# Kernel optimization log

Hardware: AMD Instinct MI355X
Metric: run time of the kernel (lower is better)

## Reference

```python
import jax, jax.numpy as jnp
import numpy as np

E = 256   # embed_dim
H = 8     # num_heads
D = E // H  # head_dim = 32
L = 1024  # seq len (Q_len == K_len == V_len)


def setup_inputs() -> dict:
    key = jax.random.key(0)
    ks = jax.random.split(key, 10)
    f = lambda k, s: jax.random.normal(k, s, dtype=jnp.float32)
    return {
        "V": f(ks[0], (L, E)),
        "K": f(ks[1], (L, E)),
        "Q": f(ks[2], (L, E)),
        # genomic-style coordinates, strictly positive
        "position": jax.random.uniform(ks[3], (L,), dtype=jnp.float32) * 1e5,
        "Wq": f(ks[4], (E, E)) * 0.02,
        "Wk": f(ks[5], (E, E)) * 0.02,
        "Wv": f(ks[6], (E, E)) * 0.02,
        "Wr": f(ks[7], (E, 1)) * 0.02,   # K_relative_linear weight [out=E, in=1]
        "Wo": f(ks[8], (E, E)) * 0.02,
        "bo": jnp.zeros((E,), jnp.float32),
    }


def reference(V, K, Q, position, Wq, Wk, Wv, Wr, Wo, bo):
    Lq = Q.shape[0]
    # projections (nn.Linear: x @ W.T), split into heads -> (L, H, D)
    q = (Q @ Wq.T).reshape(Lq, H, D)
    k = (K @ Wk.T).reshape(Lq, H, D)
    v = (V @ Wv.T).reshape(Lq, H, D)

    # relative position scalar per (q, k) pair: log(|p_q - p_k| + 1)
    rel = jnp.log(jnp.abs(position[:, None] - position[None, :]) + 1.0)  # (L, L)

    # K_relative_linear maps scalar rel -> (H, D); the einsum
    # 'nqhd,nhqjd->nhqj' then factorizes exactly as:
    #   sum_d Q[q,h,d] * rel[q,j] * Wr[h,d] = (Q . Wr)[h,q] * rel[q,j]
    # so we avoid materializing the (H, L, L, D) tensor while computing
    # mathematically identical results.
    Wr_h = Wr[:, 0].reshape(H, D)                    # (H, D)
    coeff = jnp.einsum('qhd,hd->hq', q, Wr_h)        # (H, L)

    energy = jnp.einsum('qhd,khd->hqk', q, k)        # (H, L, L)
    energy = energy + coeff[:, :, None] * rel[None, :, :]

    attn = jax.nn.softmax(energy / np.float32(E) ** 0.5, axis=2)
    out = jnp.einsum('hqk,khd->qhd', attn, v).reshape(Lq, E)
    out = out @ Wo.T + bo
    return out
```

## Files before the change

kernel.cpp:

```cpp
#include <hip/hip_runtime.h>
#include <math.h>

#define EDIM 256
#define LDIM 1024
#define HDIM 8
#define DDIM 32

typedef __attribute__((ext_vector_type(8))) short short8;
typedef __attribute__((ext_vector_type(4))) short short4v;
typedef __attribute__((ext_vector_type(4))) float f32x4;

__device__ inline unsigned short bf16h(float x) {
    unsigned u = __float_as_uint(x);
    return (unsigned short)((u + 0x7fff + ((u >> 16) & 1)) >> 16);
}
__device__ inline float bf16tof(unsigned short h) {
    return __uint_as_float(((unsigned)h) << 16);
}
__device__ inline void split8(const float4& a, const float4& b, short8& hi, short8& lo) {
    float v[8] = {a.x,a.y,a.z,a.w, b.x,b.y,b.z,b.w};
    #pragma unroll
    for (int j = 0; j < 8; ++j) {
        unsigned short hh = bf16h(v[j]);
        hi[j] = (short)hh;
        lo[j] = (short)bf16h(v[j] - bf16tof(hh));
    }
}

__global__ __launch_bounds__(256) void convertw_kernel(
    const float* __restrict__ Wq, const float* __restrict__ Wk,
    const float* __restrict__ Wv, const float* __restrict__ Wo,
    short* __restrict__ Wqh, short* __restrict__ Wql,
    short* __restrict__ Wkh, short* __restrict__ Wkl,
    short* __restrict__ Wvh, short* __restrict__ Wvl,
    short* __restrict__ Woh, short* __restrict__ Wol)
{
    const int z = blockIdx.y;
    const float* src; short* dh; short* dl;
    switch (z) {
        case 0: src = Wq; dh = Wqh; dl = Wql; break;
        case 1: src = Wk; dh = Wkh; dl = Wkl; break;
        case 2: src = Wv; dh = Wvh; dl = Wvl; break;
        default: src = Wo; dh = Woh; dl = Wol; break;
    }
    const int idx = (blockIdx.x * 256 + threadIdx.x) * 8;
    float4 a = *(const float4*)(src + idx);
    float4 b = *(const float4*)(src + idx + 4);
    short8 hi, lo;
    split8(a, b, hi, lo);
    *(short8*)&dh[idx] = hi;
    *(short8*)&dl[idx] = lo;
}

__global__ __launch_bounds__(128) void proj_kernel(
    const float* __restrict__ Q, const float* __restrict__ K, const float* __restrict__ V,
    const short* __restrict__ Wqh, const short* __restrict__ Wql,
    const short* __restrict__ Wkh, const short* __restrict__ Wkl,
    const short* __restrict__ Wvh, const short* __restrict__ Wvl,
    const float* __restrict__ Wr,
    float* __restrict__ qT, float* __restrict__ kT, float* __restrict__ vT,
    float* __restrict__ coeff)
{
    const int z = blockIdx.z;
    const float* __restrict__ X  = (z == 0) ? Q : (z == 1) ? K : V;
    const short* __restrict__ Wh = (z == 0) ? Wqh : (z == 1) ? Wkh : Wvh;
    const short* __restrict__ Wl = (z == 0) ? Wql : (z == 1) ? Wkl : Wvl;
    float* __restrict__ dst      = (z == 0) ? qT : (z == 1) ? kT : vT;

    const int n0 = blockIdx.x * 32;
    const int o0 = blockIdx.y * 64;
    const int wave = threadIdx.x >> 6;
    const int lane = threadIdx.x & 63;
    const int n16  = lane & 15;
    const int quad = lane >> 4;

    const int mrow = n0 + wave*16 + n16;

    f32x4 acc[4];
    #pragma unroll
    for (int t4 = 0; t4 < 4; ++t4) acc[t4] = (f32x4){0.f,0.f,0.f,0.f};

    #pragma unroll 2
    for (int kb = 0; kb < EDIM; kb += 32) {
        const float* xp = X + mrow*EDIM + kb + quad*8;
        float4 a0 = *(const float4*)xp;
        float4 a1 = *(const float4*)(xp + 4);
        short8 ah, al;
        split8(a0, a1, ah, al);
        #pragma unroll
        for (int t4 = 0; t4 < 4; ++t4) {
            const int orow = o0 + 16*t4 + n16;
            short8 bh = *(const short8*)&Wh[orow*EDIM + kb + quad*8];
            short8 bl = *(const short8*)&Wl[orow*EDIM + kb + quad*8];
            acc[t4] = __builtin_amdgcn_mfma_f32_16x16x32_bf16(al, bh, acc[t4], 0, 0, 0);
            acc[t4] = __builtin_amdgcn_mfma_f32_16x16x32_bf16(ah, bl, acc[t4], 0, 0, 0);
            acc[t4] = __builtin_amdgcn_mfma_f32_16x16x32_bf16(ah, bh, acc[t4], 0, 0, 0);
        }
    }

    #pragma unroll
    for (int t4 = 0; t4 < 4; ++t4) {
        const int o = o0 + 16*t4 + n16;
        const int h = o >> 5, d = o & 31;
        #pragma unroll
        for (int i = 0; i < 4; ++i) {
            const int r = n0 + wave*16 + quad*4 + i;
            dst[h*(LDIM*DDIM) + r*DDIM + d] = acc[t4][i];
        }
    }

    if (z == 0) {
        float wr[4];
        #pragma unroll
        for (int t4 = 0; t4 < 4; ++t4) wr[t4] = Wr[o0 + 16*t4 + n16];
        const int h0 = o0 >> 5;
        #pragma unroll
        for (int i = 0; i < 4; ++i) {
            float c0 = acc[0][i]*wr[0] + acc[1][i]*wr[1];
            float c1 = acc[2][i]*wr[2] + acc[3][i]*wr[3];
            #pragma unroll
            for (int off = 1; off < 16; off <<= 1) {
                c0 += __shfl_xor(c0, off, 64);
                c1 += __shfl_xor(c1, off, 64);
            }
            if (n16 == 0) {
                const int r = n0 + wave*16 + quad*4 + i;
                coeff[h0*LDIM + r]     = c0;
                coeff[(h0+1)*LDIM + r] = c1;
            }
        }
    }
}

__global__ __launch_bounds__(256, 4) void attn_kernel(
    const float* __restrict__ qT, const float* __restrict__ kT, const float* __restrict__ vT,
    const float* __restrict__ coeff, const float* __restrict__ pos,
    float* __restrict__ Op, float* __restrict__ Mp, float* __restrict__ Lp, int nkt)
{
    const int h   = blockIdx.y;
    const int q0  = blockIdx.x * 64;
    const int p   = blockIdx.z;
    const int kt0 = p * nkt * 64;
    const int tid  = threadIdx.x;
    const int wave = tid >> 6;
    const int lane = tid & 63;
    const int n    = lane & 15;
    const int quad = lane >> 4;
    const int qs0  = wave * 16;

    __shared__ __align__(16) short khi[4*64*8];
    __shared__ __align__(16) short klo[4*64*8];
    __shared__ float vs[64][36];
    __shared__ float ps_t[64][68];
    __shared__ float alph[64];
    __shared__ float pk[64];

    short8 qhi, qlo;
    {
        const float* qp = qT + (h*LDIM + q0 + qs0 + n) * DDIM + quad*8;
        float4 qa = *(const float4*)qp;
        float4 qb = *(const float4*)(qp + 4);
        split8(qa, qb, qhi, qlo);
    }

    float pq[4], cq[4];
    #pragma unroll
    for (int i = 0; i < 4; ++i) {
        const int r = q0 + qs0 + 4*quad + i;
        pq[i] = pos[r];
        cq[i] = coeff[h*LDIM + r] * 0.0625f;
    }

    float m[4], l[4];
    #pragma unroll
    for (int i = 0; i < 4; ++i) { m[i] = -INFINITY; l[i] = 0.f; }

    const int pr0 = (tid >> 4) * 4;
    const int dg2 = (tid & 15) * 2;
    float o[4][2];
    #pragma unroll
    for (int i = 0; i < 4; ++i) { o[i][0] = 0.f; o[i][1] = 0.f; }

    const int cS = tid >> 2;
    const int dq = tid & 3;
    const int lane2 = (cS & 15) | (dq << 4);
    const int gS = cS >> 4;

    float4 k0c, k1c, v0c, v1c; float pkc = 0.f;
    {
        const float* kp = kT + (h*LDIM + kt0 + cS) * DDIM + dq*8;
        k0c = *(const float4*)kp; k1c = *(const float4*)(kp + 4);
        const float* vp = vT + (h*LDIM + kt0 + cS) * DDIM + dq*8;
        v0c = *(const float4*)vp; v1c = *(const float4*)(vp + 4);
        if (tid < 64) pkc = pos[kt0 + tid];
    }

    for (int t = 0; t < nkt; ++t) {
        __syncthreads();

        {
            short8 hi8, lo8;
            split8(k0c, k1c, hi8, lo8);
            *((short8*)&khi[(gS*64 + lane2)*8]) = hi8;
            *((short8*)&klo[(gS*64 + lane2)*8]) = lo8;
            *(float4*)&vs[cS][dq*8]     = v0c;
            *(float4*)&vs[cS][dq*8 + 4] = v1c;
            if (tid < 64) pk[tid] = pkc;
        }

        float4 k0n, k1n, v0n, v1n; float pkn = 0.f;
        if (t + 1 < nkt) {
            const int kt = kt0 + (t+1) * 64;
            const float* kp = kT + (h*LDIM + kt + cS) * DDIM + dq*8;
            k0n = *(const float4*)kp; k1n = *(const float4*)(kp + 4);
            const float* vp = vT + (h*LDIM + kt + cS) * DDIM + dq*8;
            v0n = *(const float4*)vp; v1n = *(const float4*)(vp + 4);
            if (tid < 64) pkn = pos[kt + tid];
        }
        __syncthreads();

        f32x4 Sf[4];
        #pragma unroll
        for (int t4 = 0; t4 < 4; ++t4) {
            short8 bhi = *((const short8*)&khi[(t4*64 + lane)*8]);
            short8 blo = *((const short8*)&klo[(t4*64 + lane)*8]);
            f32x4 acc = {0.f, 0.f, 0.f, 0.f};
            acc = __builtin_amdgcn_mfma_f32_16x16x32_bf16(qlo, bhi, acc, 0, 0, 0);
            acc = __builtin_amdgcn_mfma_f32_16x16x32_bf16(qhi, blo, acc, 0, 0, 0);
            acc = __builtin_amdgcn_mfma_f32_16x16x32_bf16(qhi, bhi, acc, 0, 0, 0);
            Sf[t4] = acc;
        }

        float ev[4][4];
        float rmax[4] = {-INFINITY, -INFINITY, -INFINITY, -INFINITY};
        #pragma unroll
        for (int t4 = 0; t4 < 4; ++t4) {
            const float pkt = pk[16*t4 + n];
            #pragma unroll
            for (int i = 0; i < 4; ++i) {
                float s = fmaf(Sf[t4][i], 0.0625f, cq[i] * __logf(fabsf(pq[i] - pkt) + 1.f));
                ev[t4][i] = s;
                rmax[i] = fmaxf(rmax[i], s);
            }
        }
        #pragma unroll
        for (int off = 1; off < 16; off <<= 1)
            #pragma unroll
            for (int i = 0; i < 4; ++i)
                rmax[i] = fmaxf(rmax[i], __shfl_xor(rmax[i], off, 64));

        float al[4], rsum[4];
        #pragma unroll
        for (int i = 0; i < 4; ++i) {
            const float mn = fmaxf(m[i], rmax[i]);
            al[i] = __expf(m[i] - mn);
            m[i] = mn;
            rsum[i] = 0.f;
        }
        #pragma unroll
        for (int t4 = 0; t4 < 4; ++t4)
            #pragma unroll
            for (int i = 0; i < 4; ++i) {
                float e = __expf(ev[t4][i] - m[i]);
                ev[t4][i] = e;
                rsum[i] += e;
            }
        #pragma unroll
        for (int off = 1; off < 16; off <<= 1)
            #pragma unroll
            for (int i = 0; i < 4; ++i)
                rsum[i] += __shfl_xor(rsum[i], off, 64);
        #pragma unroll
        for (int i = 0; i < 4; ++i) l[i] = l[i]*al[i] + rsum[i];

        if (n == 0) {
            #pragma unroll
            for (int i = 0; i < 4; ++i) alph[qs0 + 4*quad + i] = al[i];
        }
        #pragma unroll
        for (int t4 = 0; t4 < 4; ++t4) {
            float4 w; w.x = ev[t4][0]; w.y = ev[t4][1]; w.z = ev[t4][2]; w.w = ev[t4][3];
            *(float4*)&ps_t[16*t4 + n][qs0 + 4*quad] = w;
        }
        __syncthreads();

        {
            float4 a4 = *(const float4*)&alph[pr0];
            o[0][0]*=a4.x; o[0][1]*=a4.x; o[1][0]*=a4.y; o[1][1]*=a4.y;
            o[2][0]*=a4.z; o[2][1]*=a4.z; o[3][0]*=a4.w; o[3][1]*=a4.w;
        }
        #pragma unroll 4
        for (int c = 0; c < 64; ++c) {
            float4 p4 = *(const float4*)&ps_t[c][pr0];
            float2 v2 = *(const float2*)&vs[c][dg2];
            o[0][0] += p4.x*v2.x; o[0][1] += p4.x*v2.y;
            o[1][0] += p4.y*v2.x; o[1][1] += p4.y*v2.y;
            o[2][0] += p4.z*v2.x; o[2][1] += p4.z*v2.y;
            o[3][0] += p4.w*v2.x; o[3][1] += p4.w*v2.y;
        }

        k0c = k0n; k1c = k1n; v0c = v0n; v1c = v1n; pkc = pkn;
    }

    const int ph = p * HDIM + h;
    #pragma unroll
    for (int i = 0; i < 4; ++i) {
        float2 w; w.x = o[i][0]; w.y = o[i][1];
        *(float2*)(Op + ((size_t)ph*LDIM + q0 + pr0 + i)*DDIM + dg2) = w;
    }
    if (n == 0) {
        #pragma unroll
        for (int i = 0; i < 4; ++i) {
            const int r = q0 + qs0 + 4*quad + i;
            Mp[ph*LDIM + r] = m[i];
            Lp[ph*LDIM + r] = l[i];
        }
    }
}

__global__ __launch_bounds__(256) void combine_kernel(
    const float* __restrict__ Op, const float* __restrict__ Mp, const float* __restrict__ Lp,
    int P, short* __restrict__ Ah, short* __restrict__ Al)
{
    const int idx = blockIdx.x * 256 + threadIdx.x;
    const int n  = idx >> 6;
    const int e4 = (idx & 63) * 4;
    const int h  = e4 >> 5;
    const int d  = e4 & 31;

    float mv[8], lv[8];
    float mx = -INFINITY;
    #pragma unroll
    for (int p = 0; p < 8; ++p) if (p < P) {
        mv[p] = Mp[(p*HDIM + h)*LDIM + n];
        lv[p] = Lp[(p*HDIM + h)*LDIM + n];
        mx = fmaxf(mx, mv[p]);
    }
    float s = 0.f;
    #pragma unroll
    for (int p = 0; p < 8; ++p) if (p < P) {
        float a = __expf(mv[p] - mx);
        mv[p] = a;
        s += a * lv[p];
    }
    const float inv = 1.f / s;

    float x[4] = {0.f, 0.f, 0.f, 0.f};
    #pragma unroll
    for (int p = 0; p < 8; ++p) if (p < P) {
        const float sp = mv[p] * inv;
        float4 xp = *(const float4*)(Op + ((size_t)(p*HDIM + h)*LDIM + n)*DDIM + d);
        x[0] += sp*xp.x; x[1] += sp*xp.y; x[2] += sp*xp.z; x[3] += sp*xp.w;
    }
    short4v hi, lo;
    #pragma unroll
    for (int j = 0; j < 4; ++j) {
        unsigned short hh = bf16h(x[j]);
        hi[j] = (short)hh;
        lo[j] = (short)bf16h(x[j] - bf16tof(hh));
    }
    *(short4v*)&Ah[n*EDIM + e4] = hi;
    *(short4v*)&Al[n*EDIM + e4] = lo;
}

__global__ __launch_bounds__(128) void outproj_kernel(
    const short* __restrict__ Ah, const short* __restrict__ Al,
    const short* __restrict__ Woh, const short* __restrict__ Wol,
    const float* __restrict__ bo, float* __restrict__ out)
{
    const int n0 = blockIdx.x * 32;
    const int o0 = blockIdx.y * 32;
    const int wave = threadIdx.x >> 6;
    const int lane = threadIdx.x & 63;
    const int n16  = lane & 15;
    const int quad = lane >> 4;

    const int mrow = n0 + wave*16 + n16;

    f32x4 acc[2];
    acc[0] = (f32x4){0.f,0.f,0.f,0.f};
    acc[1] = (f32x4){0.f,0.f,0.f,0.f};

    #pragma unroll 2
    for (int kb = 0; kb < EDIM; kb += 32) {
        short8 ah = *(const short8*)&Ah[mrow*EDIM + kb + quad*8];
        short8 al = *(const short8*)&Al[mrow*EDIM + kb + quad*8];
        #pragma unroll
        for (int t2 = 0; t2 < 2; ++t2) {
            const int orow = o0 + 16*t2 + n16;
            short8 bh = *(const short8*)&Woh[orow*EDIM + kb + quad*8];
            short8 bl = *(const short8*)&Wol[orow*EDIM + kb + quad*8];
            acc[t2] = __builtin_amdgcn_mfma_f32_16x16x32_bf16(al, bh, acc[t2], 0, 0, 0);
            acc[t2] = __builtin_amdgcn_mfma_f32_16x16x32_bf16(ah, bl, acc[t2], 0, 0, 0);
            acc[t2] = __builtin_amdgcn_mfma_f32_16x16x32_bf16(ah, bh, acc[t2], 0, 0, 0);
        }
    }

    #pragma unroll
    for (int t2 = 0; t2 < 2; ++t2) {
        const int o = o0 + 16*t2 + n16;
        const float b = bo[o];
        #pragma unroll
        for (int i = 0; i < 4; ++i) {
            const int r = n0 + wave*16 + quad*4 + i;
            out[r*EDIM + o] = acc[t2][i] + b;
        }
    }
}

extern "C" void kernel_launch(void* const* d_in, const int* in_sizes, int n_in,
                              void* d_out, int out_size, void* d_ws, size_t ws_size,
                              hipStream_t stream) {
    const float* V   = (const float*)d_in[0];
    const float* K   = (const float*)d_in[1];
    const float* Q   = (const float*)d_in[2];
    const float* pos = (const float*)d_in[3];
    const float* Wq  = (const float*)d_in[4];
    const float* Wk  = (const float*)d_in[5];
    const float* Wv  = (const float*)d_in[6];
    const float* Wr  = (const float*)d_in[7];
    const float* Wo  = (const float*)d_in[8];
    const float* bo  = (const float*)d_in[9];
    float* out = (float*)d_out;
    float* ws  = (float*)d_ws;

    short* Wqh = (short*)(ws);          short* Wql = (short*)(ws + 32768);
    short* Wkh = (short*)(ws + 65536);  short* Wkl = (short*)(ws + 98304);
    short* Wvh = (short*)(ws + 131072); short* Wvl = (short*)(ws + 163840);
    short* Woh = (short*)(ws + 196608); short* Wol = (short*)(ws + 229376);
    float* qT    = ws + 262144;
    float* kT    = ws + 524288;
    float* vT    = ws + 786432;
    float* coeff = ws + 1048576;
    short* Ah    = (short*)(ws + 1056768);
    short* Al    = (short*)(ws + 1187840);
    float* Op    = ws + 1319040;

    auto need = [](int P) -> size_t {
        return (size_t)(1319040 + P*278528) * 4;
    };
    int P = 2;
    if (ws_size >= need(8)) P = 8;
    else if (ws_size >= need(4)) P = 4;

    float* Mp = Op + (size_t)P * 262144;
    float* Lp = Mp + (size_t)P * 8192;

    convertw_kernel<<<dim3(32, 4),    256, 0, stream>>>(Wq, Wk, Wv, Wo,
        Wqh, Wql, Wkh, Wkl, Wvh, Wvl, Woh, Wol);
    proj_kernel    <<<dim3(32, 4, 3), 128, 0, stream>>>(Q, K, V,
        Wqh, Wql, Wkh, Wkl, Wvh, Wvl, Wr, qT, kT, vT, coeff);
    attn_kernel    <<<dim3(16, 8, P), 256, 0, stream>>>(qT, kT, vT, coeff, pos,
        Op, Mp, Lp, 16 / P);
    combine_kernel <<<dim3(256),      256, 0, stream>>>(Op, Mp, Lp, P, Ah, Al);
    outproj_kernel <<<dim3(32, 8),    128, 0, stream>>>(Ah, Al, Woh, Wol, bo, out);
}
```

Before: 124.4 us.

## Move attention PV product to split-bf16 MFMA and drop weight pre-conversion kernel

The P·V accumulation in the attention kernel moves from scalar FP32 FMAs over shared-memory tiles to three-term split-bf16 MFMA operations. V is staged in LDS as hi/lo bf16 fragments, and P is round-tripped through a row-major LDS buffer. The separate weight-conversion kernel is removed: the projection and output-projection kernels now load FP32 weights and split them inline. The combine kernel writes FP32 output, which reuses the qT buffer. This saves one launch and some memory traffic, at the cost of redundant per-block weight splitting and strided, uncoalesced V loads.

```diff
diff --git a/kernel.cpp b/kernel.cpp
--- a/kernel.cpp
+++ b/kernel.cpp
@@ -7,7 +7,6 @@
 #define DDIM 32
 
 typedef __attribute__((ext_vector_type(8))) short short8;
-typedef __attribute__((ext_vector_type(4))) short short4v;
 typedef __attribute__((ext_vector_type(4))) float f32x4;
 
 __device__ inline unsigned short bf16h(float x) {
@@ -27,45 +26,17 @@
     }
 }
 
-__global__ __launch_bounds__(256) void convertw_kernel(
-    const float* __restrict__ Wq, const float* __restrict__ Wk,
-    const float* __restrict__ Wv, const float* __restrict__ Wo,
-    short* __restrict__ Wqh, short* __restrict__ Wql,
-    short* __restrict__ Wkh, short* __restrict__ Wkl,
-    short* __restrict__ Wvh, short* __restrict__ Wvl,
-    short* __restrict__ Woh, short* __restrict__ Wol)
-{
-    const int z = blockIdx.y;
-    const float* src; short* dh; short* dl;
-    switch (z) {
-        case 0: src = Wq; dh = Wqh; dl = Wql; break;
-        case 1: src = Wk; dh = Wkh; dl = Wkl; break;
-        case 2: src = Wv; dh = Wvh; dl = Wvl; break;
-        default: src = Wo; dh = Woh; dl = Wol; break;
-    }
-    const int idx = (blockIdx.x * 256 + threadIdx.x) * 8;
-    float4 a = *(const float4*)(src + idx);
-    float4 b = *(const float4*)(src + idx + 4);
-    short8 hi, lo;
-    split8(a, b, hi, lo);
-    *(short8*)&dh[idx] = hi;
-    *(short8*)&dl[idx] = lo;
-}
-
 __global__ __launch_bounds__(128) void proj_kernel(
     const float* __restrict__ Q, const float* __restrict__ K, const float* __restrict__ V,
-    const short* __restrict__ Wqh, const short* __restrict__ Wql,
-    const short* __restrict__ Wkh, const short* __restrict__ Wkl,
-    const short* __restrict__ Wvh, const short* __restrict__ Wvl,
+    const float* __restrict__ Wq, const float* __restrict__ Wk, const float* __restrict__ Wv,
     const float* __restrict__ Wr,
     float* __restrict__ qT, float* __restrict__ kT, float* __restrict__ vT,
     float* __restrict__ coeff)
 {
     const int z = blockIdx.z;
-    const float* __restrict__ X  = (z == 0) ? Q : (z == 1) ? K : V;
-    const short* __restrict__ Wh = (z == 0) ? Wqh : (z == 1) ? Wkh : Wvh;
-    const short* __restrict__ Wl = (z == 0) ? Wql : (z == 1) ? Wkl : Wvl;
-    float* __restrict__ dst      = (z == 0) ? qT : (z == 1) ? kT : vT;
+    const float* __restrict__ X   = (z == 0) ? Q : (z == 1) ? K : V;
+    const float* __restrict__ Wfp = (z == 0) ? Wq : (z == 1) ? Wk : Wv;
+    float* __restrict__ dst       = (z == 0) ? qT : (z == 1) ? kT : vT;
 
     const int n0 = blockIdx.x * 32;
     const int o0 = blockIdx.y * 64;
@@ -85,16 +56,19 @@
         const float* xp = X + mrow*EDIM + kb + quad*8;
         float4 a0 = *(const float4*)xp;
         float4 a1 = *(const float4*)(xp + 4);
-        short8 ah, al;
-        split8(a0, a1, ah, al);
+        short8 ah, al8;
+        split8(a0, a1, ah, al8);
         #pragma unroll
         for (int t4 = 0; t4 < 4; ++t4) {
             const int orow = o0 + 16*t4 + n16;
-            short8 bh = *(const short8*)&Wh[orow*EDIM + kb + quad*8];
-            short8 bl = *(const short8*)&Wl[orow*EDIM + kb + quad*8];
-            acc[t4] = __builtin_amdgcn_mfma_f32_16x16x32_bf16(al, bh, acc[t4], 0, 0, 0);
-            acc[t4] = __builtin_amdgcn_mfma_f32_16x16x32_bf16(ah, bl, acc[t4], 0, 0, 0);
-            acc[t4] = __builtin_amdgcn_mfma_f32_16x16x32_bf16(ah, bh, acc[t4], 0, 0, 0);
+            const float* wp = Wfp + orow*EDIM + kb + quad*8;
+            float4 w0 = *(const float4*)wp;
+            float4 w1 = *(const float4*)(wp + 4);
+            short8 bh, bl;
+            split8(w0, w1, bh, bl);
+            acc[t4] = __builtin_amdgcn_mfma_f32_16x16x32_bf16(al8, bh, acc[t4], 0, 0, 0);
+            acc[t4] = __builtin_amdgcn_mfma_f32_16x16x32_bf16(ah,  bl, acc[t4], 0, 0, 0);
+            acc[t4] = __builtin_amdgcn_mfma_f32_16x16x32_bf16(ah,  bh, acc[t4], 0, 0, 0);
         }
     }
 
@@ -150,9 +124,9 @@
 
     __shared__ __align__(16) short khi[4*64*8];
     __shared__ __align__(16) short klo[4*64*8];
-    __shared__ float vs[64][36];
-    __shared__ float ps_t[64][68];
-    __shared__ float alph[64];
+    __shared__ __align__(16) short vhi[4*64*8];
+    __shared__ __align__(16) short vlo[4*64*8];
+    __shared__ float ps2[64*68];
     __shared__ float pk[64];
 
     short8 qhi, qlo;
@@ -175,23 +149,28 @@
     #pragma unroll
     for (int i = 0; i < 4; ++i) { m[i] = -INFINITY; l[i] = 0.f; }
 
-    const int pr0 = (tid >> 4) * 4;
-    const int dg2 = (tid & 15) * 2;
-    float o[4][2];
-    #pragma unroll
-    for (int i = 0; i < 4; ++i) { o[i][0] = 0.f; o[i][1] = 0.f; }
+    f32x4 od[2];
+    od[0] = (f32x4){0.f,0.f,0.f,0.f};
+    od[1] = (f32x4){0.f,0.f,0.f,0.f};
 
     const int cS = tid >> 2;
     const int dq = tid & 3;
     const int lane2 = (cS & 15) | (dq << 4);
     const int gS = cS >> 4;
-
-    float4 k0c, k1c, v0c, v1c; float pkc = 0.f;
+    const int fs  = tid >> 6;
+    const int lv  = tid & 63;
+    const int ccv = fs >> 1;
+    const int tv  = fs & 1;
+    const int cbase = ccv*32 + (lv >> 4)*8;
+    const int dv    = tv*16 + (lv & 15);
+
+    float4 k0c, k1c; float vv[8]; float pkc = 0.f;
     {
         const float* kp = kT + (h*LDIM + kt0 + cS) * DDIM + dq*8;
         k0c = *(const float4*)kp; k1c = *(const float4*)(kp + 4);
-        const float* vp = vT + (h*LDIM + kt0 + cS) * DDIM + dq*8;
-        v0c = *(const float4*)vp; v1c = *(const float4*)(vp + 4);
+        #pragma unroll
+        for (int j = 0; j < 8; ++j)
+            vv[j] = vT[(h*LDIM + kt0 + cbase + j)*DDIM + dv];
         if (tid < 64) pkc = pos[kt0 + tid];
     }
 
@@ -203,18 +182,23 @@
             split8(k0c, k1c, hi8, lo8);
             *((short8*)&khi[(gS*64 + lane2)*8]) = hi8;
             *((short8*)&klo[(gS*64 + lane2)*8]) = lo8;
-            *(float4*)&vs[cS][dq*8]     = v0c;
-            *(float4*)&vs[cS][dq*8 + 4] = v1c;
+            float4 va; va.x = vv[0]; va.y = vv[1]; va.z = vv[2]; va.w = vv[3];
+            float4 vb; vb.x = vv[4]; vb.y = vv[5]; vb.z = vv[6]; vb.w = vv[7];
+            short8 vh8, vl8;
+            split8(va, vb, vh8, vl8);
+            *((short8*)&vhi[(fs*64 + lv)*8]) = vh8;
+            *((short8*)&vlo[(fs*64 + lv)*8]) = vl8;
             if (tid < 64) pk[tid] = pkc;
         }
 
-        float4 k0n, k1n, v0n, v1n; float pkn = 0.f;
+        float4 k0n, k1n; float vvn[8]; float pkn = 0.f;
         if (t + 1 < nkt) {
             const int kt = kt0 + (t+1) * 64;
             const float* kp = kT + (h*LDIM + kt + cS) * DDIM + dq*8;
             k0n = *(const float4*)kp; k1n = *(const float4*)(kp + 4);
-            const float* vp = vT + (h*LDIM + kt + cS) * DDIM + dq*8;
-            v0n = *(const float4*)vp; v1n = *(const float4*)(vp + 4);
+            #pragma unroll
+            for (int j = 0; j < 8; ++j)
+                vvn[j] = vT[(h*LDIM + kt + cbase + j)*DDIM + dv];
             if (tid < 64) pkn = pos[kt + tid];
         }
         __syncthreads();
@@ -273,41 +257,43 @@
         #pragma unroll
         for (int i = 0; i < 4; ++i) l[i] = l[i]*al[i] + rsum[i];
 
-        if (n == 0) {
-            #pragma unroll
-            for (int i = 0; i < 4; ++i) alph[qs0 + 4*quad + i] = al[i];
-        }
-        #pragma unroll
-        for (int t4 = 0; t4 < 4; ++t4) {
-            float4 w; w.x = ev[t4][0]; w.y = ev[t4][1]; w.z = ev[t4][2]; w.w = ev[t4][3];
-            *(float4*)&ps_t[16*t4 + n][qs0 + 4*quad] = w;
-        }
-        __syncthreads();
-
-        {
-            float4 a4 = *(const float4*)&alph[pr0];
-            o[0][0]*=a4.x; o[0][1]*=a4.x; o[1][0]*=a4.y; o[1][1]*=a4.y;
-            o[2][0]*=a4.z; o[2][1]*=a4.z; o[3][0]*=a4.w; o[3][1]*=a4.w;
-        }
-        #pragma unroll 4
-        for (int c = 0; c < 64; ++c) {
-            float4 p4 = *(const float4*)&ps_t[c][pr0];
-            float2 v2 = *(const float2*)&vs[c][dg2];
-            o[0][0] += p4.x*v2.x; o[0][1] += p4.x*v2.y;
-            o[1][0] += p4.y*v2.x; o[1][1] += p4.y*v2.y;
-            o[2][0] += p4.z*v2.x; o[2][1] += p4.z*v2.y;
-            o[3][0] += p4.w*v2.x; o[3][1] += p4.w*v2.y;
-        }
-
-        k0c = k0n; k1c = k1n; v0c = v0n; v1c = v1n; pkc = pkn;
+        #pragma unroll
+        for (int t4 = 0; t4 < 4; ++t4)
+            #pragma unroll
+            for (int i = 0; i < 4; ++i)
+                ps2[(qs0 + 4*quad + i)*68 + 16*t4 + n] = ev[t4][i];
+
+        #pragma unroll
+        for (int i = 0; i < 4; ++i) { od[0][i] *= al[i]; od[1][i] *= al[i]; }
+
+        #pragma unroll
+        for (int cc = 0; cc < 2; ++cc) {
+            const float* pp = &ps2[(qs0 + n)*68 + cc*32 + quad*8];
+            float4 p0 = *(const float4*)pp;
+            float4 p1 = *(const float4*)(pp + 4);
+            short8 phi, plo;
+            split8(p0, p1, phi, plo);
+            #pragma unroll
+            for (int tt = 0; tt < 2; ++tt) {
+                short8 bvh = *((const short8*)&vhi[((cc*2 + tt)*64 + lane)*8]);
+                short8 bvl = *((const short8*)&vlo[((cc*2 + tt)*64 + lane)*8]);
+                od[tt] = __builtin_amdgcn_mfma_f32_16x16x32_bf16(plo, bvh, od[tt], 0, 0, 0);
+                od[tt] = __builtin_amdgcn_mfma_f32_16x16x32_bf16(phi, bvl, od[tt], 0, 0, 0);
+                od[tt] = __builtin_amdgcn_mfma_f32_16x16x32_bf16(phi, bvh, od[tt], 0, 0, 0);
+            }
+        }
+
+        k0c = k0n; k1c = k1n; pkc = pkn;
+        #pragma unroll
+        for (int j = 0; j < 8; ++j) vv[j] = vvn[j];
     }
 
     const int ph = p * HDIM + h;
     #pragma unroll
-    for (int i = 0; i < 4; ++i) {
-        float2 w; w.x = o[i][0]; w.y = o[i][1];
-        *(float2*)(Op + ((size_t)ph*LDIM + q0 + pr0 + i)*DDIM + dg2) = w;
-    }
+    for (int tt = 0; tt < 2; ++tt)
+        #pragma unroll
+        for (int i = 0; i < 4; ++i)
+            Op[((size_t)ph*LDIM + q0 + qs0 + 4*quad + i)*DDIM + tt*16 + n] = od[tt][i];
     if (n == 0) {
         #pragma unroll
         for (int i = 0; i < 4; ++i) {
@@ -320,7 +306,7 @@
 
 __global__ __launch_bounds__(256) void combine_kernel(
     const float* __restrict__ Op, const float* __restrict__ Mp, const float* __restrict__ Lp,
-    int P, short* __restrict__ Ah, short* __restrict__ Al)
+    int P, float* __restrict__ A)
 {
     const int idx = blockIdx.x * 256 + threadIdx.x;
     const int n  = idx >> 6;
@@ -345,27 +331,18 @@
     }
     const float inv = 1.f / s;
 
-    float x[4] = {0.f, 0.f, 0.f, 0.f};
+    float4 x; x.x = x.y = x.z = x.w = 0.f;
     #pragma unroll
     for (int p = 0; p < 8; ++p) if (p < P) {
         const float sp = mv[p] * inv;
         float4 xp = *(const float4*)(Op + ((size_t)(p*HDIM + h)*LDIM + n)*DDIM + d);
-        x[0] += sp*xp.x; x[1] += sp*xp.y; x[2] += sp*xp.z; x[3] += sp*xp.w;
-    }
-    short4v hi, lo;
-    #pragma unroll
-    for (int j = 0; j < 4; ++j) {
-        unsigned short hh = bf16h(x[j]);
-        hi[j] = (short)hh;
-        lo[j] = (short)bf16h(x[j] - bf16tof(hh));
-    }
-    *(short4v*)&Ah[n*EDIM + e4] = hi;
-    *(short4v*)&Al[n*EDIM + e4] = lo;
+        x.x += sp*xp.x; x.y += sp*xp.y; x.z += sp*xp.z; x.w += sp*xp.w;
+    }
+    *(float4*)(A + n*EDIM + e4) = x;
 }
 
 __global__ __launch_bounds__(128) void outproj_kernel(
-    const short* __restrict__ Ah, const short* __restrict__ Al,
-    const short* __restrict__ Woh, const short* __restrict__ Wol,
+    const float* __restrict__ A, const float* __restrict__ Wo,
     const float* __restrict__ bo, float* __restrict__ out)
 {
     const int n0 = blockIdx.x * 32;
@@ -383,16 +360,22 @@
 
     #pragma unroll 2
     for (int kb = 0; kb < EDIM; kb += 32) {
-        short8 ah = *(const short8*)&Ah[mrow*EDIM + kb + quad*8];
-        short8 al = *(const short8*)&Al[mrow*EDIM + kb + quad*8];
+        const float* ap = A + mrow*EDIM + kb + quad*8;
+        float4 a0 = *(const float4*)ap;
+        float4 a1 = *(const float4*)(ap + 4);
+        short8 ah, al8;
+        split8(a0, a1, ah, al8);
         #pragma unroll
         for (int t2 = 0; t2 < 2; ++t2) {
             const int orow = o0 + 16*t2 + n16;
-            short8 bh = *(const short8*)&Woh[orow*EDIM + kb + quad*8];
-            short8 bl = *(const short8*)&Wol[orow*EDIM + kb + quad*8];
-            acc[t2] = __builtin_amdgcn_mfma_f32_16x16x32_bf16(al, bh, acc[t2], 0, 0, 0);
-            acc[t2] = __builtin_amdgcn_mfma_f32_16x16x32_bf16(ah, bl, acc[t2], 0, 0, 0);
-            acc[t2] = __builtin_amdgcn_mfma_f32_16x16x32_bf16(ah, bh, acc[t2], 0, 0, 0);
+            const float* wp = Wo + orow*EDIM + kb + quad*8;
+            float4 w0 = *(const float4*)wp;
+            float4 w1 = *(const float4*)(wp + 4);
+            short8 bh, bl;
+            split8(w0, w1, bh, bl);
+            acc[t2] = __builtin_amdgcn_mfma_f32_16x16x32_bf16(al8, bh, acc[t2], 0, 0, 0);
+            acc[t2] = __builtin_amdgcn_mfma_f32_16x16x32_bf16(ah,  bl, acc[t2], 0, 0, 0);
+            acc[t2] = __builtin_amdgcn_mfma_f32_16x16x32_bf16(ah,  bh, acc[t2], 0, 0, 0);
         }
     }
 
@@ -424,20 +407,14 @@
     float* out = (float*)d_out;
     float* ws  = (float*)d_ws;
 
-    short* Wqh = (short*)(ws);          short* Wql = (short*)(ws + 32768);
-    short* Wkh = (short*)(ws + 65536);  short* Wkl = (short*)(ws + 98304);
-    short* Wvh = (short*)(ws + 131072); short* Wvl = (short*)(ws + 163840);
-    short* Woh = (short*)(ws + 196608); short* Wol = (short*)(ws + 229376);
-    float* qT    = ws + 262144;
-    float* kT    = ws + 524288;
-    float* vT    = ws + 786432;
-    float* coeff = ws + 1048576;
-    short* Ah    = (short*)(ws + 1056768);
-    short* Al    = (short*)(ws + 1187840);
-    float* Op    = ws + 1319040;
+    float* qT    = ws;
+    float* kT    = ws + 262144;
+    float* vT    = ws + 524288;
+    float* coeff = ws + 786432;
+    float* Op    = ws + 794624;
 
     auto need = [](int P) -> size_t {
-        return (size_t)(1319040 + P*278528) * 4;
+        return (size_t)(794624 + P*278528) * 4;
     };
     int P = 2;
     if (ws_size >= need(8)) P = 8;
@@ -445,13 +422,12 @@
 
     float* Mp = Op + (size_t)P * 262144;
     float* Lp = Mp + (size_t)P * 8192;
-
-    convertw_kernel<<<dim3(32, 4),    256, 0, stream>>>(Wq, Wk, Wv, Wo,
-        Wqh, Wql, Wkh, Wkl, Wvh, Wvl, Woh, Wol);
-    proj_kernel    <<<dim3(32, 4, 3), 128, 0, stream>>>(Q, K, V,
-        Wqh, Wql, Wkh, Wkl, Wvh, Wvl, Wr, qT, kT, vT, coeff);
+    float* A  = qT;
+
+    proj_kernel    <<<dim3(32, 4, 3), 128, 0, stream>>>(Q, K, V, Wq, Wk, Wv, Wr,
+                                                        qT, kT, vT, coeff);
     attn_kernel    <<<dim3(16, 8, P), 256, 0, stream>>>(qT, kT, vT, coeff, pos,
-        Op, Mp, Lp, 16 / P);
-    combine_kernel <<<dim3(256),      256, 0, stream>>>(Op, Mp, Lp, P, Ah, Al);
-    outproj_kernel <<<dim3(32, 8),    128, 0, stream>>>(Ah, Al, Woh, Wol, bo, out);
-}
+                                                        Op, Mp, Lp, 16 / P);
+    combine_kernel <<<dim3(256),      256, 0, stream>>>(Op, Mp, Lp, P, A);
+    outproj_kernel <<<dim3(32, 8),    128, 0, stream>>>(A, Wo, bo, out);
+}
```

Result: no change. 126.8 us (+1.9%).
